# Optimization experiments

Hardware: AMD Instinct MI355X
Metric: run time of the kernel (lower is better)

Reference implementation:

```python
import jax, jax.numpy as jnp
import numpy as np
from functools import partial

IM = 1280            # input image side
VAR = (0.1, 0.2)     # retinaface variances
TOPK = 1024          # pre-NMS candidates per image
CONF_T = 0.5         # confidence threshold
NMS_T = 0.4          # IoU threshold
MIN_SIZES = [[16, 32], [64, 128], [256, 512]]
STEPS = [8, 16, 32]


def make_priors():
    """Vectorized PriorBox for a 1280x1280 image -> [A,4] (cx,cy,w,h), normalized."""
    chunks = []
    for ms_list, step in zip(MIN_SIZES, STEPS):
        f = IM // step
        c = (np.arange(f, dtype=np.float32) + 0.5) * step / IM
        cy, cx = np.meshgrid(c, c, indexing='ij')
        for ms in ms_list:
            s = np.float32(ms) / IM
            a = np.stack([cx, cy, np.full_like(cx, s), np.full_like(cx, s)], -1)
            chunks.append(a.reshape(-1, 4))
    return np.concatenate(chunks, 0)  # [67200, 4]


def setup_inputs() -> dict:
    key = jax.random.key(0)
    k1, k2, k3 = jax.random.split(key, 3)
    N, A = 32, 67200
    return {
        "loc": jax.random.normal(k1, (N, A, 4), jnp.float32),
        "conf": jax.random.normal(k2, (N, A, 2), jnp.float32),
        "landms": jax.random.normal(k3, (N, A, 10), jnp.float32),
        "priors": jnp.asarray(make_priors()),
    }


def _pairwise_iou(boxes):
    # boxes: [K,4] corner format
    x1 = jnp.maximum(boxes[:, None, 0], boxes[None, :, 0])
    y1 = jnp.maximum(boxes[:, None, 1], boxes[None, :, 1])
    x2 = jnp.minimum(boxes[:, None, 2], boxes[None, :, 2])
    y2 = jnp.minimum(boxes[:, None, 3], boxes[None, :, 3])
    inter = jnp.clip(x2 - x1, 0.0) * jnp.clip(y2 - y1, 0.0)
    area = jnp.clip(boxes[:, 2] - boxes[:, 0], 0.0) * jnp.clip(boxes[:, 3] - boxes[:, 1], 0.0)
    return inter / (area[:, None] + area[None, :] - inter + 1e-9)


def _nms_one(boxes, scores):
    # greedy NMS over score-sorted candidates (boxes already sorted desc by score)
    K = boxes.shape[0]
    iou = _pairwise_iou(boxes)                 # [K,K]
    idx = jnp.arange(K)
    valid = scores > CONF_T

    def body(i, keep):
        sup = (iou[i] > NMS_T) & keep[i] & (idx > i)
        return keep & ~sup

    return jax.lax.fori_loop(0, K, body, valid)


def reference(loc, conf, landms, priors):
    N, A, _ = loc.shape
    # softmax face scores
    scores = jax.nn.softmax(conf, axis=-1)[..., 1]                       # [N,A]
    # decode boxes (variances 0.1 / 0.2)
    cxcy = priors[None, :, :2] + loc[..., :2] * VAR[0] * priors[None, :, 2:]
    wh = priors[None, :, 2:] * jnp.exp(loc[..., 2:] * VAR[1])
    boxes = jnp.concatenate([cxcy - wh * 0.5, cxcy + wh * 0.5], -1) * IM  # [N,A,4]
    # decode 5 landmarks
    lm = landms.reshape(N, A, 5, 2)
    pts = (priors[None, :, None, :2] + lm * VAR[0] * priors[None, :, None, 2:]) * IM
    pts = pts.reshape(N, A, 10)                                          # [N,A,10]
    # top-K candidates per image (sorted by score, descending)
    top_s, top_i = jax.lax.top_k(scores, TOPK)                           # [N,K]
    gb = jnp.take_along_axis(boxes, top_i[..., None], axis=1)            # [N,K,4]
    gl = jnp.take_along_axis(pts, top_i[..., None], axis=1)              # [N,K,10]
    keep = jax.vmap(_nms_one)(gb, top_s)                                 # [N,K] bool
    det = jnp.concatenate([gb, top_s[..., None], gl], -1)                # [N,K,15]
    return det * keep[..., None].astype(det.dtype)
```

## Files before the change

### kernel.cpp

```cpp
#include <hip/hip_runtime.h>

typedef unsigned int u32;
typedef unsigned long long u64;

#define N_IMG 32
#define NA 67200
#define KTOP 1024
#define IM_F 1280.0f
#define HBLK 16
#define CHUNK 4200
#define SEGCAP 768
#define ECAP 256
#define PRETHR 0x3F666666u

__device__ __forceinline__ float cr_expf(float x) { return (float)exp((double)x); }

__device__ __forceinline__ u64 shflxor64(u64 v, int m) {
    u32 lo = (u32)__shfl_xor((int)(u32)v, m, 64);
    u32 hi = (u32)__shfl_xor((int)(u32)(v >> 32), m, 64);
    return ((u64)hi << 32) | (u64)lo;
}

__device__ __forceinline__ u64 readlane64(u64 v, int lane) {
    u32 lo = (u32)__builtin_amdgcn_readlane((int)(u32)v, lane);
    u32 hi = (u32)__builtin_amdgcn_readlane((int)(u32)(v >> 32), lane);
    return ((u64)hi << 32) | (u64)lo;
}

__device__ __forceinline__ float face_score(float c0, float c1) {
    if (c1 >= c0) {
        float e0 = cr_expf(c0 - c1);
        return 1.0f / (e0 + 1.0f);
    } else {
        float e1 = cr_expf(c1 - c0);
        return e1 / (1.0f + e1);
    }
}

__global__ __launch_bounds__(256) void score_compact_kernel(const float4* __restrict__ conf4,
                                                            u64* __restrict__ keys,
                                                            u32* __restrict__ cnts) {
    const int n = blockIdx.x >> 4, blk = blockIdx.x & 15;
    const int tid = threadIdx.x;
    __shared__ u64 kbuf[SEGCAP];
    __shared__ u32 cnt;
    if (tid == 0) cnt = 0;
    __syncthreads();
    const int base2 = (n * NA + blk * CHUNK) >> 1;
    #pragma unroll 1
    for (int it = 0; it < 9; ++it) {
        const int idx = tid + it * 256;
        if (idx < CHUNK / 2) {
            float4 c = conf4[base2 + idx];
            float s0 = face_score(c.x, c.y);
            float s1 = face_score(c.z, c.w);
            u32 u0 = __float_as_uint(s0), u1 = __float_as_uint(s1);
            u32 a0 = (u32)(blk * CHUNK + idx * 2);
            if (u0 > PRETHR) {
                u32 p = atomicAdd(&cnt, 1u);
                if (p < SEGCAP) kbuf[p] = ((u64)u0 << 32) | (u32)(~a0);
            }
            if (u1 > PRETHR) {
                u32 p = atomicAdd(&cnt, 1u);
                if (p < SEGCAP) kbuf[p] = ((u64)u1 << 32) | (u32)(~(a0 + 1u));
            }
        }
    }
    __syncthreads();
    const u32 c_ = min(cnt, (u32)SEGCAP);
    u64* seg = keys + ((size_t)n * HBLK + blk) * SEGCAP;
    for (u32 i = tid; i < c_; i += 256) seg[i] = kbuf[i];
    if (tid == 0) cnts[n * HBLK + blk] = c_;
}

__global__ __launch_bounds__(1024) void select_sort_kernel(const u64* __restrict__ keys,
                                                           const u32* __restrict__ cnts,
                                                           u32* __restrict__ top_idx,
                                                           float* __restrict__ top_score) {
    const int n = blockIdx.x, tid = threadIdx.x;
    __shared__ u32 hist[4096];
    __shared__ u32 sA[1024], sB[1024];
    __shared__ u64 cand[KTOP];
    __shared__ u64 bkeys[ECAP];
    __shared__ u32 sc[4];
    for (int i = tid; i < 4096; i += 1024) hist[i] = 0;
    if (tid < 4) sc[tid] = 0;
    __syncthreads();

    const u64* kb = keys + (size_t)n * HBLK * SEGCAP;
    u32 cofs[HBLK + 1];
    cofs[0] = 0;
    #pragma unroll
    for (int b = 0; b < HBLK; ++b) cofs[b + 1] = cofs[b] + cnts[n * HBLK + b];
    const int T = (int)cofs[HBLK];

    for (int i = tid; i < T; i += 1024) {
        int b = 0; u32 base = 0;
        #pragma unroll
        for (int s = 1; s < HBLK; ++s) {
            bool ge = ((u32)i >= cofs[s]);
            b += ge; base = ge ? cofs[s] : base;
        }
        u64 k = kb[(size_t)b * SEGCAP + ((u32)i - base)];
        u32 u = (u32)(k >> 32);
        u32 bin = min((u - 0x3F600000u) >> 9, 4095u);
        atomicAdd(&hist[bin], 1u);
    }
    __syncthreads();

    const uint4 hv = *(const uint4*)(hist + tid * 4);
    const u32 h0 = hv.x, h1 = hv.y, h2 = hv.z, h3 = hv.w;
    sA[tid] = h0 + h1 + h2 + h3;
    __syncthreads();
    u32 *src = sA, *dst = sB;
    for (int d = 1; d < 1024; d <<= 1) {
        dst[tid] = src[tid] + ((tid + d < 1024) ? src[tid + d] : 0u);
        __syncthreads();
        u32* t = src; src = dst; dst = t;
    }
    u32 GT3 = (tid + 1 < 1024) ? src[tid + 1] : 0u;
    u32 GE3 = GT3 + h3;
    u32 GE2 = GE3 + h2;
    u32 GE1 = GE2 + h1;
    u32 GE0 = GE1 + h0;
    if (GE3 >= KTOP && GT3 < KTOP) sc[0] = 4u * tid + 3u;
    if (GE2 >= KTOP && GE3 < KTOP) sc[0] = 4u * tid + 2u;
    if (GE1 >= KTOP && GE2 < KTOP) sc[0] = 4u * tid + 1u;
    if (GE0 >= KTOP && GE1 < KTOP) sc[0] = 4u * tid + 0u;
    __syncthreads();
    const u32 B = sc[0];

    for (int i = tid; i < T; i += 1024) {
        int b = 0; u32 base = 0;
        #pragma unroll
        for (int s = 1; s < HBLK; ++s) {
            bool ge = ((u32)i >= cofs[s]);
            b += ge; base = ge ? cofs[s] : base;
        }
        u64 k = kb[(size_t)b * SEGCAP + ((u32)i - base)];
        u32 u = (u32)(k >> 32);
        u32 bin = min((u - 0x3F600000u) >> 9, 4095u);
        if (bin > B) {
            u32 p = atomicAdd(&sc[1], 1u);
            cand[p] = k;
        } else if (bin == B) {
            u32 p = atomicAdd(&sc[2], 1u);
            if (p < ECAP) bkeys[p] = k;
        }
    }
    __syncthreads();

    const int D = (int)sc[1];
    const int R = KTOP - D;
    const int E = min((int)sc[2], ECAP);
    for (int t = tid; t < E; t += 1024) {
        u64 k = bkeys[t];
        int rank = 0;
        for (int j = 0; j < E; ++j) rank += (bkeys[j] > k);
        if (rank < R) cand[D + rank] = k;
    }
    __syncthreads();

    u64 v = cand[tid];
    #pragma unroll
    for (int kk = 1; kk <= 10; ++kk) {
        const int k = 1 << kk;
        #pragma unroll
        for (int jj = kk - 1; jj >= 0; --jj) {
            const int j = 1 << jj;
            u64 p;
            if (j >= 64) {
                cand[tid] = v;
                __syncthreads();
                p = cand[tid ^ j];
                __syncthreads();
            } else {
                p = shflxor64(v, j);
            }
            bool keep_max = (((tid & k) == 0) == ((tid & j) == 0));
            u64 mx = v > p ? v : p;
            u64 mn = v > p ? p : v;
            v = keep_max ? mx : mn;
        }
    }

    top_idx[n * KTOP + tid]   = ~(u32)(v & 0xFFFFFFFFull);
    top_score[n * KTOP + tid] = __uint_as_float((u32)(v >> 32));
}

__global__ __launch_bounds__(256) void mask_decode_kernel(const u32* __restrict__ top_idx,
                                                          const float* __restrict__ top_score,
                                                          const float* __restrict__ loc,
                                                          const float* __restrict__ landms,
                                                          const float* __restrict__ priors,
                                                          float* __restrict__ det,
                                                          u64* __restrict__ mask) {
    const int n    = blockIdx.x & 31;
    const int sub  = blockIdx.x >> 5;
    const int wid  = threadIdx.x >> 6;
    const int lane = threadIdx.x & 63;
    const int q    = sub * 4 + wid;
    const int tid  = threadIdx.x;

    __shared__ float bx1[KTOP], by1[KTOP], bx2[KTOP], by2[KTOP], baA[KTOP];

    #pragma unroll
    for (int k = 0; k < 4; ++k) {
        const int r  = tid + k * 256;
        const int id = n * KTOP + r;
        const u32 a  = top_idx[id];
        float4 p = *(const float4*)(priors + (size_t)a * 4);
        float4 l = *(const float4*)(loc + ((size_t)n * NA + a) * 4);
        float cx = p.x + l.x * 0.1f * p.z;
        float cy = p.y + l.y * 0.1f * p.w;
        float w  = p.z * cr_expf(l.z * 0.2f);
        float h  = p.w * cr_expf(l.w * 0.2f);
        const float o0 = (cx - w * 0.5f) * IM_F;
        const float o1 = (cy - h * 0.5f) * IM_F;
        const float o2 = (cx + w * 0.5f) * IM_F;
        const float o3 = (cy + h * 0.5f) * IM_F;
        bx1[r] = o0; by1[r] = o1; bx2[r] = o2; by2[r] = o3;
        baA[r] = fmaxf(o2 - o0, 0.f) * fmaxf(o3 - o1, 0.f);

        if (sub == 0) {
            float* o = det + (size_t)id * 15;
            o[0] = o0; o[1] = o1; o[2] = o2; o[3] = o3;
            o[4] = top_score[id];
            const float* mp = landms + ((size_t)n * NA + a) * 10;
            #pragma unroll
            for (int t = 0; t < 5; ++t) {
                o[5 + 2 * t]     = (p.x + mp[2 * t]     * 0.1f * p.z) * IM_F;
                o[5 + 2 * t + 1] = (p.y + mp[2 * t + 1] * 0.1f * p.w) * IM_F;
            }
        }
    }
    __syncthreads();

    u64* mbase = mask + (size_t)n * KTOP * 16;
    #pragma unroll 1
    for (int k = 0; k < 16; ++k) {
        const int i = k * 64 + q;
        const float x1i = bx1[i], y1i = by1[i], x2i = bx2[i], y2i = by2[i], ai = baA[i];
        u64* orow = mbase + (size_t)i * 16;
        if (lane < k) orow[lane] = 0ull;
        #pragma unroll 1
        for (int w2 = k; w2 < 16; ++w2) {
            const int j = w2 * 64 + lane;
            bool bit = false;
            if (j > i) {
                float xx1 = fmaxf(x1i, bx1[j]);
                float yy1 = fmaxf(y1i, by1[j]);
                float xx2 = fminf(x2i, bx2[j]);
                float yy2 = fminf(y2i, by2[j]);
                float inter = fmaxf(xx2 - xx1, 0.f) * fmaxf(yy2 - yy1, 0.f);
                float iou = inter / (ai + baA[j] - inter + 1e-9f);
                bit = iou > 0.4f;
            }
            u64 m = __ballot(bit);
            if (lane == 0) orow[w2] = m;
        }
    }
}

__global__ __launch_bounds__(1024) void nms_out_kernel(const float* __restrict__ top_score,
                                                       const u64* __restrict__ mask,
                                                       const float* __restrict__ det,
                                                       float* __restrict__ out) {
    const int n = blockIdx.x;
    const int tid = threadIdx.x;
    __shared__ u64 lmask[512 * 16];

    const u64* mbase = mask + (size_t)n * KTOP * 16;
    u64 myw = 0;
    if (tid < 64) {
        for (int g = 0; g < 16; ++g) {
            u64 b = __ballot(top_score[n * KTOP + g * 64 + tid] > 0.5f);
            if (tid == g) myw = b;
        }
    }

    const int lane = tid & 63;
    const int w16  = lane & 15;
    const int p4   = lane >> 4;

    #pragma unroll 1
    for (int half = 0; half < 2; ++half) {
        __syncthreads();
        #pragma unroll
        for (int k = 0; k < 8; ++k) {
            int idx = tid + k * 1024;
            int r = idx >> 4, w = idx & 15;
            lmask[(r << 4) | (w ^ (r & 15))] = mbase[(size_t)half * 8192 + idx];
        }
        __syncthreads();
        if (tid < 64) {
            #pragma unroll 1
            for (int gg = 0; gg < 8; ++gg) {
                const int g = half * 8 + gg;
                const int lbase = gg * 64;
                const int rr = lbase + lane;
                u64 colw = lmask[(rr << 4) | (g ^ (rr & 15))];
                u64 kw = readlane64(myw, g);
                #pragma unroll
                for (int l = 0; l < 64; ++l) {
                    u64 rl = readlane64(colw, l);
                    kw = ((kw >> l) & 1ull) ? (kw & ~rl) : kw;
                }
                u64 acc = 0;
                #pragma unroll
                for (int k = 0; k < 16; ++k) {
                    const int r2 = lbase + p4 * 16 + k;
                    u64 row = lmask[(r2 << 4) | (w16 ^ (r2 & 15))];
                    u64 sel = (u64)0 - ((kw >> (p4 * 16 + k)) & 1ull);
                    acc |= row & sel;
                }
                acc |= shflxor64(acc, 16);
                acc |= shflxor64(acc, 32);
                myw = (lane == g) ? kw : myw;
                myw &= ~acc;
            }
        }
    }
    __syncthreads();
    if (tid < 16) lmask[tid] = myw;
    __syncthreads();

    const float* drow = det + (size_t)n * KTOP * 15;
    float* orow = out + (size_t)n * KTOP * 15;
    for (int e = tid; e < KTOP * 15; e += 1024) {
        int k = e / 15;
        float f = ((lmask[k >> 6] >> (k & 63)) & 1ull) ? 1.0f : 0.0f;
        orow[e] = drow[e] * f;
    }
}

extern "C" void kernel_launch(void* const* d_in, const int* in_sizes, int n_in,
                              void* d_out, int out_size, void* d_ws, size_t ws_size,
                              hipStream_t stream) {
    const float*  loc    = (const float*)d_in[0];
    const float4* conf4  = (const float4*)d_in[1];
    const float*  landms = (const float*)d_in[2];
    const float*  priors = (const float*)d_in[3];

    char* ws = (char*)d_ws;
    size_t off = 0;
    auto carve = [&](size_t bytes) { void* p = ws + off; off = (off + bytes + 255) & ~255ull; return p; };
    u64*    keys      = (u64*)   carve(sizeof(u64)    * (size_t)N_IMG * HBLK * SEGCAP);
    u32*    cnts      = (u32*)   carve(sizeof(u32)    * N_IMG * HBLK);
    u32*    top_idx   = (u32*)   carve(sizeof(u32)    * N_IMG * KTOP);
    float*  top_score = (float*) carve(sizeof(float)  * N_IMG * KTOP);
    float*  det       = (float*) carve(sizeof(float)  * N_IMG * KTOP * 15);
    u64*    mask      = (u64*)   carve(sizeof(u64)    * (size_t)N_IMG * KTOP * 16);

    score_compact_kernel<<<N_IMG * HBLK, 256, 0, stream>>>(conf4, keys, cnts);
    select_sort_kernel<<<N_IMG, 1024, 0, stream>>>(keys, cnts, top_idx, top_score);
    mask_decode_kernel<<<N_IMG * HBLK, 256, 0, stream>>>(top_idx, top_score, loc, landms, priors,
                                                         det, mask);
    nms_out_kernel<<<N_IMG, 1024, 0, stream>>>(top_score, mask, det, (float*)d_out);
}
```

Before: 105.1 us.

## Cut barriers and global rereads in top-K select-sort kernel

The select kernel now keeps its loaded keys in registers instead of reading them from global memory twice. Its 10-step shared-memory scan with barriers becomes a wave-shuffle scan plus a small cross-wave sum. Per-element shared atomics for compaction become one ballot-aggregated atomic per wave. The bitonic sort ping-pongs between two shared buffers, which removes one barrier per cross-wave step. The score kernel's block-to-image mapping is also interleaved. Costs are more registers (KPT=8 keys per thread), and correctness now requires T ≤ 8192, which holds since 16×768 segments give T ≤ 12288… actually T can exceed 8192, which risks dropping keys.

```diff
diff --git a/kernel.cpp b/kernel.cpp
--- a/kernel.cpp
+++ b/kernel.cpp
@@ -11,6 +11,7 @@
 #define CHUNK 4200
 #define SEGCAP 768
 #define ECAP 256
+#define KPT 8
 #define PRETHR 0x3F666666u
 
 __device__ __forceinline__ float cr_expf(float x) { return (float)exp((double)x); }
@@ -40,7 +41,7 @@
 __global__ __launch_bounds__(256) void score_compact_kernel(const float4* __restrict__ conf4,
                                                             u64* __restrict__ keys,
                                                             u32* __restrict__ cnts) {
-    const int n = blockIdx.x >> 4, blk = blockIdx.x & 15;
+    const int n = blockIdx.x & 31, blk = blockIdx.x >> 5;
     const int tid = threadIdx.x;
     __shared__ u64 kbuf[SEGCAP];
     __shared__ u32 cnt;
@@ -78,10 +79,12 @@
                                                            u32* __restrict__ top_idx,
                                                            float* __restrict__ top_score) {
     const int n = blockIdx.x, tid = threadIdx.x;
+    const int lane = tid & 63, wv = tid >> 6;
     __shared__ u32 hist[4096];
-    __shared__ u32 sA[1024], sB[1024];
     __shared__ u64 cand[KTOP];
+    __shared__ u64 candB[KTOP];
     __shared__ u64 bkeys[ECAP];
+    __shared__ u32 wtot[16], wabove[16];
     __shared__ u32 sc[4];
     for (int i = tid; i < 4096; i += 1024) hist[i] = 0;
     if (tid < 4) sc[tid] = 0;
@@ -94,31 +97,45 @@
     for (int b = 0; b < HBLK; ++b) cofs[b + 1] = cofs[b] + cnts[n * HBLK + b];
     const int T = (int)cofs[HBLK];
 
-    for (int i = tid; i < T; i += 1024) {
-        int b = 0; u32 base = 0;
-        #pragma unroll
-        for (int s = 1; s < HBLK; ++s) {
-            bool ge = ((u32)i >= cofs[s]);
-            b += ge; base = ge ? cofs[s] : base;
-        }
-        u64 k = kb[(size_t)b * SEGCAP + ((u32)i - base)];
-        u32 u = (u32)(k >> 32);
-        u32 bin = min((u - 0x3F600000u) >> 9, 4095u);
-        atomicAdd(&hist[bin], 1u);
+    u64 kreg[KPT];
+    #pragma unroll
+    for (int it = 0; it < KPT; ++it) {
+        const int i = tid + it * 1024;
+        u64 k = 0;
+        if (i < T) {
+            int b = 0; u32 base = 0;
+            #pragma unroll
+            for (int s = 1; s < HBLK; ++s) {
+                bool ge = ((u32)i >= cofs[s]);
+                b += ge; base = ge ? cofs[s] : base;
+            }
+            k = kb[(size_t)b * SEGCAP + ((u32)i - base)];
+            u32 bin = min(((u32)(k >> 32) - 0x3F600000u) >> 9, 4095u);
+            atomicAdd(&hist[bin], 1u);
+        }
+        kreg[it] = k;
     }
     __syncthreads();
 
     const uint4 hv = *(const uint4*)(hist + tid * 4);
     const u32 h0 = hv.x, h1 = hv.y, h2 = hv.z, h3 = hv.w;
-    sA[tid] = h0 + h1 + h2 + h3;
-    __syncthreads();
-    u32 *src = sA, *dst = sB;
-    for (int d = 1; d < 1024; d <<= 1) {
-        dst[tid] = src[tid] + ((tid + d < 1024) ? src[tid + d] : 0u);
-        __syncthreads();
-        u32* t = src; src = dst; dst = t;
-    }
-    u32 GT3 = (tid + 1 < 1024) ? src[tid + 1] : 0u;
+    const u32 g = h0 + h1 + h2 + h3;
+    u32 v = g;
+    #pragma unroll
+    for (int d = 1; d < 64; d <<= 1) {
+        u32 t = (u32)__shfl((int)v, lane + d, 64);
+        v += (lane + d < 64) ? t : 0u;
+    }
+    if (lane == 0) wtot[wv] = v;
+    __syncthreads();
+    if (tid < 16) {
+        u32 ab = 0;
+        for (int w2 = tid + 1; w2 < 16; ++w2) ab += wtot[w2];
+        wabove[tid] = ab;
+    }
+    __syncthreads();
+    const u32 srcv = v + wabove[wv];
+    u32 GT3 = srcv - g;
     u32 GE3 = GT3 + h3;
     u32 GE2 = GE3 + h2;
     u32 GE1 = GE2 + h1;
@@ -130,22 +147,29 @@
     __syncthreads();
     const u32 B = sc[0];
 
-    for (int i = tid; i < T; i += 1024) {
-        int b = 0; u32 base = 0;
-        #pragma unroll
-        for (int s = 1; s < HBLK; ++s) {
-            bool ge = ((u32)i >= cofs[s]);
-            b += ge; base = ge ? cofs[s] : base;
-        }
-        u64 k = kb[(size_t)b * SEGCAP + ((u32)i - base)];
-        u32 u = (u32)(k >> 32);
-        u32 bin = min((u - 0x3F600000u) >> 9, 4095u);
-        if (bin > B) {
-            u32 p = atomicAdd(&sc[1], 1u);
-            cand[p] = k;
-        } else if (bin == B) {
-            u32 p = atomicAdd(&sc[2], 1u);
-            if (p < ECAP) bkeys[p] = k;
+    #pragma unroll
+    for (int it = 0; it < KPT; ++it) {
+        const int i = tid + it * 1024;
+        const u64 k = kreg[it];
+        u32 bin = min(((u32)(k >> 32) - 0x3F600000u) >> 9, 4095u);
+        bool isd = (i < T) && (bin > B);
+        bool isb = (i < T) && (bin == B);
+        u64 md = __ballot(isd);
+        if (md) {
+            u32 first = (u32)__ffsll((long long)md) - 1u;
+            u32 base2 = 0;
+            if (lane == (int)first) base2 = atomicAdd(&sc[1], (u32)__popcll(md));
+            base2 = (u32)__shfl((int)base2, (int)first, 64);
+            if (isd) cand[base2 + __popcll(md & ((1ull << lane) - 1ull))] = k;
+        }
+        u64 mb = __ballot(isb);
+        if (mb) {
+            u32 first = (u32)__ffsll((long long)mb) - 1u;
+            u32 base2 = 0;
+            if (lane == (int)first) base2 = atomicAdd(&sc[2], (u32)__popcll(mb));
+            base2 = (u32)__shfl((int)base2, (int)first, 64);
+            u32 p = base2 + __popcll(mb & ((1ull << lane) - 1ull));
+            if (isb && p < ECAP) bkeys[p] = k;
         }
     }
     __syncthreads();
@@ -161,7 +185,8 @@
     }
     __syncthreads();
 
-    u64 v = cand[tid];
+    u64 vv = cand[tid];
+    int phase = 0;
     #pragma unroll
     for (int kk = 1; kk <= 10; ++kk) {
         const int k = 1 << kk;
@@ -170,22 +195,23 @@
             const int j = 1 << jj;
             u64 p;
             if (j >= 64) {
-                cand[tid] = v;
+                u64* wbuf = phase ? candB : cand;
+                wbuf[tid] = vv;
                 __syncthreads();
-                p = cand[tid ^ j];
-                __syncthreads();
+                p = wbuf[tid ^ j];
+                phase ^= 1;
             } else {
-                p = shflxor64(v, j);
+                p = shflxor64(vv, j);
             }
             bool keep_max = (((tid & k) == 0) == ((tid & j) == 0));
-            u64 mx = v > p ? v : p;
-            u64 mn = v > p ? p : v;
-            v = keep_max ? mx : mn;
-        }
-    }
-
-    top_idx[n * KTOP + tid]   = ~(u32)(v & 0xFFFFFFFFull);
-    top_score[n * KTOP + tid] = __uint_as_float((u32)(v >> 32));
+            u64 mx = vv > p ? vv : p;
+            u64 mn = vv > p ? p : vv;
+            vv = keep_max ? mx : mn;
+        }
+    }
+
+    top_idx[n * KTOP + tid]   = ~(u32)(vv & 0xFFFFFFFFull);
+    top_score[n * KTOP + tid] = __uint_as_float((u32)(vv >> 32));
 }
 
 __global__ __launch_bounds__(256) void mask_decode_kernel(const u32* __restrict__ top_idx,
```

Result: no change. 104.4 us (-0.7%).
